# Kernel optimization log

Measured on AMD Instinct MI355X. Metric: run time of the kernel, lower is better.

The kernel has to match this reference:

```python
import jax, jax.numpy as jnp
import numpy as np

N = 100000      # nodes
E = 1600000     # edges (avg degree 16)
F_IN = 64       # in_channels
H = 64          # hidden_channels
L = 3           # num_layers
FINAL = H * L   # jk='cat'


def setup_inputs() -> dict:
    key = jax.random.key(0)
    ks = jax.random.split(key, 16)

    def w(k, i, o):
        return (jax.random.normal(k, (i, o), jnp.float32) / np.sqrt(i)).astype(jnp.float32)

    x = jax.random.normal(ks[0], (N, F_IN), jnp.float32)
    edge_index = jax.random.randint(ks[1], (2, E), 0, N, dtype=jnp.int32)

    inp = {
        'x': x,
        'edge_index': edge_index,
        # layer 1 (in -> H): lin_l (neighbors, with bias), lin_r (root, no bias)
        'W1l': w(ks[2], F_IN, H), 'b1': jnp.zeros((H,), jnp.float32), 'W1r': w(ks[3], F_IN, H),
        # layer 2 (H -> H)
        'W2l': w(ks[4], H, H), 'b2': jnp.zeros((H,), jnp.float32), 'W2r': w(ks[5], H, H),
        # layer 3 (H -> H)
        'W3l': w(ks[6], H, H), 'b3': jnp.zeros((H,), jnp.float32), 'W3r': w(ks[7], H, H),
        # final linear on JK-concat
        'Wlin': w(ks[8], FINAL, 1), 'blin': jnp.zeros((1,), jnp.float32),
    }
    return inp


def _sage_conv(x, src, dst, inv_deg, Wl, bl, Wr):
    # gather neighbor features along edges, segment-mean by destination node
    msg = x[src]                                             # [E, F]
    agg = jax.ops.segment_sum(msg, dst, num_segments=N)      # [N, F]
    agg = agg * inv_deg[:, None]                             # mean aggregation
    return agg @ Wl + bl + x @ Wr                            # lin_l(agg) + lin_r(x)


def reference(x, edge_index, W1l, b1, W1r, W2l, b2, W2r, W3l, b3, W3r, Wlin, blin):
    src, dst = edge_index[0], edge_index[1]
    deg = jax.ops.segment_sum(jnp.ones((E,), jnp.float32), dst, num_segments=N)
    inv_deg = 1.0 / jnp.maximum(deg, 1.0)

    xs = []
    h = x
    for (Wl, bl, Wr) in ((W1l, b1, W1r), (W2l, b2, W2r), (W3l, b3, W3r)):
        h = jax.nn.relu(_sage_conv(h, src, dst, inv_deg, Wl, bl, Wr))
        # dropout is identity in eval mode
        xs.append(h)

    hcat = jnp.concatenate(xs, axis=-1)   # JK 'cat' -> [N, H*L]
    out = hcat @ Wlin + blin              # [N, 1]
    return jax.nn.sigmoid(out).reshape(-1)
```

## Files before the change

kernel.cpp:

```cpp
#include <hip/hip_runtime.h>
#include <math.h>

#define N_NODES 100000
#define N_EDGES 1600000
#define HD 64
#define TILE 128
#define NBUCK 128
#define BNODES 1024
#define EPB 4096
#define EPB2 8192
#define HB 196

typedef unsigned short ushort_t;
typedef unsigned char uchar_t;
typedef __attribute__((ext_vector_type(8))) unsigned short ushort8_t;
typedef __attribute__((ext_vector_type(8))) short short8_t;
typedef __attribute__((ext_vector_type(4))) float float4_t;
typedef __attribute__((ext_vector_type(2))) float float2_t;

__device__ __forceinline__ float bf2f(ushort_t h){
  union{unsigned u; float f;} v; v.u = ((unsigned)h)<<16; return v.f;
}
__device__ __forceinline__ ushort_t f2bf(float f){
  union{float f; unsigned u;} v; v.f=f;
  unsigned b = v.u + 0x7FFF + ((v.u>>16)&1);
  return (ushort_t)(b>>16);
}
__device__ __forceinline__ void acc8(float* acc, unsigned ux, unsigned uy, float m){
  float2_t f;
  f=__builtin_amdgcn_cvt_pk_f32_fp8((int)ux,false); acc[0]=fmaf(m,f.x,acc[0]); acc[1]=fmaf(m,f.y,acc[1]);
  f=__builtin_amdgcn_cvt_pk_f32_fp8((int)ux,true ); acc[2]=fmaf(m,f.x,acc[2]); acc[3]=fmaf(m,f.y,acc[3]);
  f=__builtin_amdgcn_cvt_pk_f32_fp8((int)uy,false); acc[4]=fmaf(m,f.x,acc[4]); acc[5]=fmaf(m,f.y,acc[5]);
  f=__builtin_amdgcn_cvt_pk_f32_fp8((int)uy,true ); acc[6]=fmaf(m,f.x,acc[6]); acc[7]=fmaf(m,f.y,acc[7]);
}

__global__ __launch_bounds__(512) void k_convert_hist(
    const float* __restrict__ in, ushort_t* __restrict__ obf, uchar_t* __restrict__ o8,
    const int* __restrict__ dst, int* __restrict__ bcnt2d, int nfeat, int nedge){
  __shared__ int lh[NBUCK];
  int t=threadIdx.x, b=blockIdx.x;
  bool doHist = (b < HB);
  if(doHist){
    if(t<NBUCK) lh[t]=0;
    __syncthreads();
    int base=b*EPB2;
    #pragma unroll
    for(int j=0;j<16;j++){
      int e=base+t+j*512;
      if(e<nedge) atomicAdd(&lh[dst[e]>>10],1);
    }
  }
  int idx = (b*512+t)*4;
  if(idx+3<nfeat){
    float4 v = *(const float4*)&in[idx];
    ushort2 a; a.x=f2bf(v.x); a.y=f2bf(v.y);
    ushort2 c2; c2.x=f2bf(v.z); c2.y=f2bf(v.w);
    *(ushort2*)&obf[idx] = a;
    *(ushort2*)&obf[idx+2] = c2;
    int p = __builtin_amdgcn_cvt_pk_fp8_f32(v.x, v.y, 0, false);
    p     = __builtin_amdgcn_cvt_pk_fp8_f32(v.z, v.w, p, true);
    *(unsigned int*)&o8[idx] = (unsigned int)p;
  } else {
    for(int k=idx;k<nfeat;k++){
      obf[k]=f2bf(in[k]);
      int p = __builtin_amdgcn_cvt_pk_fp8_f32(in[k], 0.f, 0, false);
      o8[k] = (uchar_t)(p & 0xFF);
    }
  }
  if(doHist){
    __syncthreads();
    if(t<NBUCK) bcnt2d[b*NBUCK+t]=lh[t];
  }
}

__global__ void k_scan128(const int* __restrict__ bcnt2d, int* __restrict__ gcur, int* __restrict__ gbase){
  __shared__ int s[NBUCK];
  int t=threadIdx.x;
  int v=0;
  int b=0;
  for(; b+4<=HB; b+=4)
    v += bcnt2d[b*NBUCK+t] + bcnt2d[(b+1)*NBUCK+t] + bcnt2d[(b+2)*NBUCK+t] + bcnt2d[(b+3)*NBUCK+t];
  for(; b<HB; ++b) v += bcnt2d[b*NBUCK+t];
  s[t]=v;
  __syncthreads();
  for(int off=1; off<NBUCK; off<<=1){
    int a=(t>=off)? s[t-off]:0;
    __syncthreads();
    s[t]+=a;
    __syncthreads();
  }
  int excl = s[t]-v;
  gcur[t]=excl;
  gbase[t]=excl;
  if(t==NBUCK-1) gbase[NBUCK]=s[t];
}

__global__ __launch_bounds__(512) void k_reorder(
    const int* __restrict__ src, const int* __restrict__ dst,
    int* __restrict__ gcur, int* __restrict__ pairs, int n){
  __shared__ int lh[NBUCK];
  __shared__ int lbase[NBUCK];
  int t=threadIdx.x;
  if(t<NBUCK) lh[t]=0;
  __syncthreads();
  int base = blockIdx.x*EPB;
  int bb[8], rr[8], pv[8];
  #pragma unroll
  for(int j=0;j<8;j++){
    int e = base + t + j*512;
    if(e<n){
      int d=dst[e];
      int b=d>>10;
      rr[j]=atomicAdd(&lh[b],1);
      bb[j]=b;
      pv[j]=src[e] | ((d & 1023)<<17);
    } else bb[j]=-1;
  }
  __syncthreads();
  if(t<NBUCK && lh[t]) lbase[t]=atomicAdd(&gcur[t], lh[t]);
  __syncthreads();
  #pragma unroll
  for(int j=0;j<8;j++){
    if(bb[j]>=0){
      int pos = lbase[bb[j]] + rr[j];
      pairs[pos] = pv[j];
    }
  }
}

__global__ __launch_bounds__(512) void k_bucket_csr(
    const int* __restrict__ pairs, const int* __restrict__ gbase,
    int* __restrict__ rowptr, float* __restrict__ invdeg,
    int* __restrict__ csr, int nnodes, int nedges){
  __shared__ int cnt[BNODES];
  __shared__ int part[512];
  int t=threadIdx.x, b=blockIdx.x;
  int nb0 = b*BNODES;
  int e0 = gbase[b], e1 = gbase[b+1];
  cnt[t]=0; cnt[t+512]=0;
  __syncthreads();
  for(int e=e0+t; e<e1; e+=512) atomicAdd(&cnt[pairs[e]>>17], 1);
  __syncthreads();
  int c0 = cnt[2*t], c1 = cnt[2*t+1];
  part[t] = c0+c1;
  __syncthreads();
  for(int off=1; off<512; off<<=1){
    int a=(t>=off)? part[t-off]:0;
    __syncthreads();
    part[t]+=a;
    __syncthreads();
  }
  int base = part[t]-(c0+c1);
  int ex0 = base, ex1 = base+c0;
  int n_0 = nb0+2*t, n_1 = nb0+2*t+1;
  if(n_0<nnodes){ rowptr[n_0]=e0+ex0; invdeg[n_0]=1.0f/fmaxf((float)c0,1.0f); }
  if(n_1<nnodes){ rowptr[n_1]=e0+ex1; invdeg[n_1]=1.0f/fmaxf((float)c1,1.0f); }
  if(b==0 && t==0) rowptr[nnodes]=nedges;
  cnt[2*t]=ex0; cnt[2*t+1]=ex1;
  __syncthreads();
  for(int e=e0+t; e<e1; e+=512){
    int p = pairs[e];
    int pos = atomicAdd(&cnt[p>>17], 1);
    csr[e0+pos] = p & 0x1FFFF;
  }
}

__global__ __launch_bounds__(512) void k_gather(
    const uchar_t* __restrict__ hin8, ushort_t* __restrict__ agg,
    const int* __restrict__ rowptr, const int* __restrict__ csr,
    const float* __restrict__ invdeg, int nnodes)
{
  int t=threadIdx.x;
  int lane=t&63, wid=t>>6;
  int nA=(blockIdx.x*8+wid)*2;
  if(nA>=nnodes) return;
  int nB=nA+1;
  bool hasB = (nB<nnodes);
  int slot=lane>>3, c=lane&7;
  int rA0=rowptr[nA], rA1=rowptr[nA+1];
  int rB0=rA1, rB1=hasB? rowptr[nB+1] : rA1;
  float idgA=invdeg[nA];
  float idgB=hasB? invdeg[nB] : 0.f;
  float aA[8]={0,0,0,0,0,0,0,0}, aB[8]={0,0,0,0,0,0,0,0};
  int ca=(rA1>rA0)? rA1-1 : 0;
  int cb=(rB1>rB0)? rB1-1 : 0;

  {
    int i1=rA0+slot, i2=rA0+8+slot;
    int j1=rB0+slot, j2=rB0+8+slot;
    int sA1=csr[min(i1,ca)], sA2=csr[min(i2,ca)];
    int sB1=csr[min(j1,cb)], sB2=csr[min(j2,cb)];
    uint2 uA1=*(const uint2*)&hin8[(size_t)sA1*HD + c*8];
    uint2 uA2=*(const uint2*)&hin8[(size_t)sA2*HD + c*8];
    uint2 uB1=*(const uint2*)&hin8[(size_t)sB1*HD + c*8];
    uint2 uB2=*(const uint2*)&hin8[(size_t)sB2*HD + c*8];
    acc8(aA,uA1.x,uA1.y,(i1<rA1)?1.f:0.f);
    acc8(aA,uA2.x,uA2.y,(i2<rA1)?1.f:0.f);
    acc8(aB,uB1.x,uB1.y,(j1<rB1)?1.f:0.f);
    acc8(aB,uB2.x,uB2.y,(j2<rB1)?1.f:0.f);
  }
  int eA=rA0+16, eB=rB0+16;
  for(; eA<rA1 && eB<rB1; eA+=16, eB+=16){
    int i1=eA+slot, i2=eA+8+slot;
    int j1=eB+slot, j2=eB+8+slot;
    int sA1=csr[min(i1,ca)], sA2=csr[min(i2,ca)];
    int sB1=csr[min(j1,cb)], sB2=csr[min(j2,cb)];
    uint2 uA1=*(const uint2*)&hin8[(size_t)sA1*HD + c*8];
    uint2 uA2=*(const uint2*)&hin8[(size_t)sA2*HD + c*8];
    uint2 uB1=*(const uint2*)&hin8[(size_t)sB1*HD + c*8];
    uint2 uB2=*(const uint2*)&hin8[(size_t)sB2*HD + c*8];
    acc8(aA,uA1.x,uA1.y,(i1<rA1)?1.f:0.f);
    acc8(aA,uA2.x,uA2.y,(i2<rA1)?1.f:0.f);
    acc8(aB,uB1.x,uB1.y,(j1<rB1)?1.f:0.f);
    acc8(aB,uB2.x,uB2.y,(j2<rB1)?1.f:0.f);
  }
  for(; eA<rA1; eA+=16){
    int i1=eA+slot, i2=eA+8+slot;
    int s1=csr[min(i1,ca)], s2=csr[min(i2,ca)];
    uint2 u1=*(const uint2*)&hin8[(size_t)s1*HD + c*8];
    uint2 u2=*(const uint2*)&hin8[(size_t)s2*HD + c*8];
    acc8(aA,u1.x,u1.y,(i1<rA1)?1.f:0.f);
    acc8(aA,u2.x,u2.y,(i2<rA1)?1.f:0.f);
  }
  for(; eB<rB1; eB+=16){
    int i1=eB+slot, i2=eB+8+slot;
    int s1=csr[min(i1,cb)], s2=csr[min(i2,cb)];
    uint2 u1=*(const uint2*)&hin8[(size_t)s1*HD + c*8];
    uint2 u2=*(const uint2*)&hin8[(size_t)s2*HD + c*8];
    acc8(aB,u1.x,u1.y,(i1<rB1)?1.f:0.f);
    acc8(aB,u2.x,u2.y,(i2<rB1)?1.f:0.f);
  }
  #pragma unroll
  for(int off=8; off<64; off<<=1){
    #pragma unroll
    for(int j=0;j<8;j++){
      aA[j] += __shfl_xor(aA[j], off, 64);
      aB[j] += __shfl_xor(aB[j], off, 64);
    }
  }
  if(slot==0){
    ushort8_t o;
    #pragma unroll
    for(int j=0;j<8;j++) o[j] = f2bf(aA[j]*idgA);
    *(ushort8_t*)&agg[(size_t)nA*HD + c*8] = o;
    if(hasB){
      #pragma unroll
      for(int j=0;j<8;j++) o[j] = f2bf(aB[j]*idgB);
      *(ushort8_t*)&agg[(size_t)nB*HD + c*8] = o;
    }
  }
}

__global__ __launch_bounds__(256) void k_dense(
    const ushort_t* __restrict__ hin, const ushort_t* __restrict__ agg,
    ushort_t* __restrict__ hout, uchar_t* __restrict__ h8out,
    const float* __restrict__ Wl, const float* __restrict__ bvec, const float* __restrict__ Wr,
    const float* __restrict__ wseg, const float* __restrict__ blin,
    float* __restrict__ partial, float* __restrict__ finout,
    int first, int nnodes)
{
  __shared__ ushort_t sWt[64][136];
  __shared__ ushort_t sOut[TILE][72];
  __shared__ float sB[64], sS[64];
  int t = threadIdx.x;
  int n0 = blockIdx.x*TILE;

  {
    int col = t & 63;
    int k0  = (t >> 6) * 32;
    #pragma unroll
    for (int j = 0; j < 32; ++j) {
      int k = k0 + j;
      float wv = (k < 64) ? Wl[k*64 + col] : Wr[(k-64)*64 + col];
      sWt[col][k] = f2bf(wv);
    }
  }
  if(t<64){ sB[t]=bvec[t]; sS[t]=wseg[t]; }
  __syncthreads();

  int lane = t & 63, wv_ = t >> 6;
  int r16 = lane & 15, g4 = lane >> 4;
  int nbase = n0 + wv_*32;

  float4_t acc[2][4];
  #pragma unroll
  for(int mt=0;mt<2;mt++)
    #pragma unroll
    for(int ct=0;ct<4;ct++)
      #pragma unroll
      for(int r=0;r<4;r++) acc[mt][ct][r]=0.f;

  #pragma unroll
  for (int ks = 0; ks < 4; ++ks) {
    const ushort_t* abuf = (ks < 2) ? agg : hin;
    int koff = (ks & 1)*32 + g4*8;
    short8_t aF[2];
    #pragma unroll
    for (int mt = 0; mt < 2; ++mt) {
      int node = nbase + mt*16 + r16;
      if (node >= nnodes) node = nnodes-1;
      aF[mt] = *(const short8_t*)&abuf[(size_t)node*HD + koff];
    }
    #pragma unroll
    for (int ct = 0; ct < 4; ++ct) {
      short8_t bF = *(const short8_t*)&sWt[ct*16 + r16][ks*32 + g4*8];
      acc[0][ct] = __builtin_amdgcn_mfma_f32_16x16x32_bf16(aF[0], bF, acc[0][ct], 0,0,0);
      acc[1][ct] = __builtin_amdgcn_mfma_f32_16x16x32_bf16(aF[1], bF, acc[1][ct], 0,0,0);
    }
  }

  #pragma unroll
  for (int mt = 0; mt < 2; ++mt)
    #pragma unroll
    for (int ct = 0; ct < 4; ++ct) {
      int col = ct*16 + r16;
      #pragma unroll
      for (int r = 0; r < 4; ++r) {
        int row = g4*4 + r;
        float v = fmaxf(acc[mt][ct][r] + sB[col], 0.f);
        sOut[wv_*32 + mt*16 + row][col] = f2bf(v);
      }
    }
  __syncthreads();

  {
    int nl = t >> 1, half = t & 1;
    int node = n0 + nl;
    float p = 0.f;
    #pragma unroll
    for (int i = 0; i < 4; ++i) {
      int c0 = half*32 + i*8;
      ushort8_t v = *(const ushort8_t*)&sOut[nl][c0];
      float fv[8];
      #pragma unroll
      for (int j = 0; j < 8; ++j){ fv[j]=bf2f(v[j]); p = fmaf(fv[j], sS[c0+j], p); }
      if (!finout && node < nnodes){
        *(ushort8_t*)&hout[(size_t)node*HD + c0] = v;
        int q0 = __builtin_amdgcn_cvt_pk_fp8_f32(fv[0], fv[1], 0, false);
        q0     = __builtin_amdgcn_cvt_pk_fp8_f32(fv[2], fv[3], q0, true);
        int q1 = __builtin_amdgcn_cvt_pk_fp8_f32(fv[4], fv[5], 0, false);
        q1     = __builtin_amdgcn_cvt_pk_fp8_f32(fv[6], fv[7], q1, true);
        uint2 st; st.x=(unsigned)q0; st.y=(unsigned)q1;
        *(uint2*)&h8out[(size_t)node*HD + c0] = st;
      }
    }
    p += __shfl_xor(p, 1, 64);
    if (half == 0 && node < nnodes) {
      float q = first ? (blin[0] + p) : (partial[node] + p);
      if (finout) finout[node] = 1.0f/(1.0f+expf(-q));
      else partial[node] = q;
    }
  }
}

extern "C" void kernel_launch(void* const* d_in, const int* in_sizes, int n_in,
                              void* d_out, int out_size, void* d_ws, size_t ws_size,
                              hipStream_t stream){
  const float* x    =(const float*)d_in[0];
  const int*   ei   =(const int*)  d_in[1];
  const float* W1l  =(const float*)d_in[2];
  const float* b1   =(const float*)d_in[3];
  const float* W1r  =(const float*)d_in[4];
  const float* W2l  =(const float*)d_in[5];
  const float* b2   =(const float*)d_in[6];
  const float* W2r  =(const float*)d_in[7];
  const float* W3l  =(const float*)d_in[8];
  const float* b3   =(const float*)d_in[9];
  const float* W3r  =(const float*)d_in[10];
  const float* Wlin =(const float*)d_in[11];
  const float* blin =(const float*)d_in[12];
  float* out=(float*)d_out;

  const int N=N_NODES, E=N_EDGES;
  char* ws=(char*)d_ws;
  size_t off=0;
  auto take=[&](size_t bytes)->char*{ char* p=ws+off; off=(off+bytes+255)&~(size_t)255; return p; };
  int*      bcnt2d   =(int*)     take((size_t)HB*NBUCK*4);
  int*      gcur     =(int*)     take((size_t)NBUCK*4);
  int*      gbase    =(int*)     take((size_t)(NBUCK+1)*4);
  int*      rowptr   =(int*)     take((size_t)(N+1)*4);
  int*      csr      =(int*)     take((size_t)E*4);
  int*      pairs    =(int*)     take((size_t)E*4);
  float*    invdeg   =(float*)   take((size_t)N*4);
  ushort_t* xbf      =(ushort_t*)take((size_t)N*HD*2);
  ushort_t* hbfA     =(ushort_t*)take((size_t)N*HD*2);
  ushort_t* hbfB     =(ushort_t*)take((size_t)N*HD*2);
  ushort_t* aggbf    =(ushort_t*)take((size_t)N*HD*2);
  uchar_t*  x8       =(uchar_t*) take((size_t)N*HD);
  uchar_t*  h8A      =(uchar_t*) take((size_t)N*HD);
  uchar_t*  h8B      =(uchar_t*) take((size_t)N*HD);
  float*    pacc     =(float*)   take((size_t)N*4);

  const int RB=(E+EPB-1)/EPB;
  const int CB=(N*HD/4+511)/512;
  const int BB=(N+BNODES-1)/BNODES;

  k_convert_hist<<<CB, 512, 0, stream>>>(x, xbf, x8, ei+E, bcnt2d, N*HD, E);
  k_scan128     <<<1, NBUCK, 0, stream>>>(bcnt2d, gcur, gbase);
  k_reorder     <<<RB, 512, 0, stream>>>(ei, ei+E, gcur, pairs, E);
  k_bucket_csr  <<<BB, 512, 0, stream>>>(pairs, gbase, rowptr, invdeg, csr, N, E);

  dim3 gg((N+15)/16);
  dim3 gd((N+TILE-1)/TILE);

  k_gather<<<gg, 512, 0, stream>>>(x8,  aggbf, rowptr, csr, invdeg, N);
  k_dense <<<gd, 256, 0, stream>>>(xbf,  aggbf, hbfA, h8A, W1l,b1,W1r, Wlin+0,   blin, pacc, (float*)nullptr, 1, N);
  k_gather<<<gg, 512, 0, stream>>>(h8A, aggbf, rowptr, csr, invdeg, N);
  k_dense <<<gd, 256, 0, stream>>>(hbfA, aggbf, hbfB, h8B, W2l,b2,W2r, Wlin+64,  blin, pacc, (float*)nullptr, 0, N);
  k_gather<<<gg, 512, 0, stream>>>(h8B, aggbf, rowptr, csr, invdeg, N);
  k_dense <<<gd, 256, 0, stream>>>(hbfB, aggbf, hbfA, h8A, W3l,b3,W3r, Wlin+128, blin, pacc, out, 0, N);
}
```

Measured before the change: 196.8 us.

## Fuse neighbor gather with dense SAGE layer and pre-convert weights once

Merges the per-layer gather kernel and the dense MFMA kernel into one kernel. Each 512-thread block aggregates 16 nodes into shared memory, then four waves run the 16-row bf16 MFMA, apply ReLU and the JK partial dot. This removes the global round trip for the aggregated features and three kernel launches. Weight transposition and bf16 conversion move to a single prep kernel that writes all layers once, so blocks only copy them into shared memory. In exchange, each small block reloads 16KB of weights, and only 4 of 8 waves do MFMA work.

```diff
diff --git a/kernel.cpp b/kernel.cpp
--- a/kernel.cpp
+++ b/kernel.cpp
@@ -4,7 +4,6 @@
 #define N_NODES 100000
 #define N_EDGES 1600000
 #define HD 64
-#define TILE 128
 #define NBUCK 128
 #define BNODES 1024
 #define EPB 4096
@@ -14,6 +13,7 @@
 typedef unsigned short ushort_t;
 typedef unsigned char uchar_t;
 typedef __attribute__((ext_vector_type(8))) unsigned short ushort8_t;
+typedef __attribute__((ext_vector_type(4))) unsigned short ushort4_t;
 typedef __attribute__((ext_vector_type(8))) short short8_t;
 typedef __attribute__((ext_vector_type(4))) float float4_t;
 typedef __attribute__((ext_vector_type(2))) float float2_t;
@@ -73,6 +73,26 @@
   }
 }
 
+__global__ void k_prep_w(const float* __restrict__ W1l, const float* __restrict__ W1r,
+                         const float* __restrict__ W2l, const float* __restrict__ W2r,
+                         const float* __restrict__ W3l, const float* __restrict__ W3r,
+                         ushort_t* __restrict__ wt){
+  int idx = blockIdx.x*512 + threadIdx.x;
+  int layer = idx>>11;
+  int rem = idx & 2047;
+  int col = rem >> 5;
+  int kg = rem & 31;
+  const float* Wl = layer==0? W1l : (layer==1? W2l : W3l);
+  const float* Wr = layer==0? W1r : (layer==1? W2r : W3r);
+  ushort_t* o = wt + layer*8192 + col*128 + kg*4;
+  #pragma unroll
+  for(int i=0;i<4;i++){
+    int k = kg*4+i;
+    float v = (k<64)? Wl[k*64+col] : Wr[(k-64)*64+col];
+    o[i]=f2bf(v);
+  }
+}
+
 __global__ void k_scan128(const int* __restrict__ bcnt2d, int* __restrict__ gcur, int* __restrict__ gbase){
   __shared__ int s[NBUCK];
   int t=threadIdx.x;
@@ -165,190 +185,158 @@
   }
 }
 
-__global__ __launch_bounds__(512) void k_gather(
-    const uchar_t* __restrict__ hin8, ushort_t* __restrict__ agg,
-    const int* __restrict__ rowptr, const int* __restrict__ csr,
-    const float* __restrict__ invdeg, int nnodes)
+__global__ __launch_bounds__(512) void k_fused(
+    const ushort_t* __restrict__ hin, const uchar_t* __restrict__ hin8,
+    const ushort_t* __restrict__ wt,
+    const float* __restrict__ bvec, const float* __restrict__ wseg, const float* __restrict__ blin,
+    const int* __restrict__ rowptr, const int* __restrict__ csr, const float* __restrict__ invdeg,
+    ushort_t* __restrict__ hout, uchar_t* __restrict__ h8out,
+    float* __restrict__ pacc, float* __restrict__ finout, int first, int nnodes)
 {
+  __shared__ __align__(16) ushort_t sWt[64][136];
+  __shared__ __align__(16) ushort_t sAgg[16][72];
+  __shared__ __align__(16) ushort_t sOut[16][72];
+  __shared__ float sB[64], sS[64];
   int t=threadIdx.x;
-  int lane=t&63, wid=t>>6;
-  int nA=(blockIdx.x*8+wid)*2;
-  if(nA>=nnodes) return;
-  int nB=nA+1;
-  bool hasB = (nB<nnodes);
-  int slot=lane>>3, c=lane&7;
-  int rA0=rowptr[nA], rA1=rowptr[nA+1];
-  int rB0=rA1, rB1=hasB? rowptr[nB+1] : rA1;
-  float idgA=invdeg[nA];
-  float idgB=hasB? invdeg[nB] : 0.f;
-  float aA[8]={0,0,0,0,0,0,0,0}, aB[8]={0,0,0,0,0,0,0,0};
-  int ca=(rA1>rA0)? rA1-1 : 0;
-  int cb=(rB1>rB0)? rB1-1 : 0;
+  int n0=blockIdx.x*16;
 
   {
-    int i1=rA0+slot, i2=rA0+8+slot;
-    int j1=rB0+slot, j2=rB0+8+slot;
-    int sA1=csr[min(i1,ca)], sA2=csr[min(i2,ca)];
-    int sB1=csr[min(j1,cb)], sB2=csr[min(j2,cb)];
-    uint2 uA1=*(const uint2*)&hin8[(size_t)sA1*HD + c*8];
-    uint2 uA2=*(const uint2*)&hin8[(size_t)sA2*HD + c*8];
-    uint2 uB1=*(const uint2*)&hin8[(size_t)sB1*HD + c*8];
-    uint2 uB2=*(const uint2*)&hin8[(size_t)sB2*HD + c*8];
-    acc8(aA,uA1.x,uA1.y,(i1<rA1)?1.f:0.f);
-    acc8(aA,uA2.x,uA2.y,(i2<rA1)?1.f:0.f);
-    acc8(aB,uB1.x,uB1.y,(j1<rB1)?1.f:0.f);
-    acc8(aB,uB2.x,uB2.y,(j2<rB1)?1.f:0.f);
-  }
-  int eA=rA0+16, eB=rB0+16;
-  for(; eA<rA1 && eB<rB1; eA+=16, eB+=16){
-    int i1=eA+slot, i2=eA+8+slot;
-    int j1=eB+slot, j2=eB+8+slot;
-    int sA1=csr[min(i1,ca)], sA2=csr[min(i2,ca)];
-    int sB1=csr[min(j1,cb)], sB2=csr[min(j2,cb)];
-    uint2 uA1=*(const uint2*)&hin8[(size_t)sA1*HD + c*8];
-    uint2 uA2=*(const uint2*)&hin8[(size_t)sA2*HD + c*8];
-    uint2 uB1=*(const uint2*)&hin8[(size_t)sB1*HD + c*8];
-    uint2 uB2=*(const uint2*)&hin8[(size_t)sB2*HD + c*8];
-    acc8(aA,uA1.x,uA1.y,(i1<rA1)?1.f:0.f);
-    acc8(aA,uA2.x,uA2.y,(i2<rA1)?1.f:0.f);
-    acc8(aB,uB1.x,uB1.y,(j1<rB1)?1.f:0.f);
-    acc8(aB,uB2.x,uB2.y,(j2<rB1)?1.f:0.f);
-  }
-  for(; eA<rA1; eA+=16){
-    int i1=eA+slot, i2=eA+8+slot;
-    int s1=csr[min(i1,ca)], s2=csr[min(i2,ca)];
-    uint2 u1=*(const uint2*)&hin8[(size_t)s1*HD + c*8];
-    uint2 u2=*(const uint2*)&hin8[(size_t)s2*HD + c*8];
-    acc8(aA,u1.x,u1.y,(i1<rA1)?1.f:0.f);
-    acc8(aA,u2.x,u2.y,(i2<rA1)?1.f:0.f);
-  }
-  for(; eB<rB1; eB+=16){
-    int i1=eB+slot, i2=eB+8+slot;
-    int s1=csr[min(i1,cb)], s2=csr[min(i2,cb)];
-    uint2 u1=*(const uint2*)&hin8[(size_t)s1*HD + c*8];
-    uint2 u2=*(const uint2*)&hin8[(size_t)s2*HD + c*8];
-    acc8(aB,u1.x,u1.y,(i1<rB1)?1.f:0.f);
-    acc8(aB,u2.x,u2.y,(i2<rB1)?1.f:0.f);
-  }
-  #pragma unroll
-  for(int off=8; off<64; off<<=1){
+    int col=t>>3, sub=t&7;
+    const ushort8_t* src=(const ushort8_t*)(wt + col*128);
+    ushort8_t* dst=(ushort8_t*)&sWt[col][0];
+    dst[sub*2]   = src[sub*2];
+    dst[sub*2+1] = src[sub*2+1];
+  }
+  if(t<64){ sB[t]=bvec[t]; sS[t]=wseg[t]; }
+
+  {
+    int lane=t&63, wid=t>>6;
+    int nA=n0+wid*2, nB=nA+1;
+    if(nA<nnodes){
+      bool hasB=(nB<nnodes);
+      int slot=lane>>3, c=lane&7;
+      int rA0=rowptr[nA], rA1=rowptr[nA+1];
+      int rB0=rA1, rB1=hasB? rowptr[nB+1] : rA1;
+      float idgA=invdeg[nA];
+      float idgB=hasB? invdeg[nB] : 0.f;
+      float aA[8]={0,0,0,0,0,0,0,0}, aB[8]={0,0,0,0,0,0,0,0};
+      int ca=(rA1>rA0)? rA1-1 : 0;
+      int cb=(rB1>rB0)? rB1-1 : 0;
+      {
+        int i1=rA0+slot, i2=rA0+8+slot;
+        int j1=rB0+slot, j2=rB0+8+slot;
+        int sA1=csr[min(i1,ca)], sA2=csr[min(i2,ca)];
+        int sB1=csr[min(j1,cb)], sB2=csr[min(j2,cb)];
+        uint2 uA1=*(const uint2*)&hin8[(size_t)sA1*HD + c*8];
+        uint2 uA2=*(const uint2*)&hin8[(size_t)sA2*HD + c*8];
+        uint2 uB1=*(const uint2*)&hin8[(size_t)sB1*HD + c*8];
+        uint2 uB2=*(const uint2*)&hin8[(size_t)sB2*HD + c*8];
+        acc8(aA,uA1.x,uA1.y,(i1<rA1)?1.f:0.f);
+        acc8(aA,uA2.x,uA2.y,(i2<rA1)?1.f:0.f);
+        acc8(aB,uB1.x,uB1.y,(j1<rB1)?1.f:0.f);
+        acc8(aB,uB2.x,uB2.y,(j2<rB1)?1.f:0.f);
+      }
+      int eA=rA0+16, eB=rB0+16;
+      for(; eA<rA1 && eB<rB1; eA+=16, eB+=16){
+        int i1=eA+slot, i2=eA+8+slot;
+        int j1=eB+slot, j2=eB+8+slot;
+        int sA1=csr[min(i1,ca)], sA2=csr[min(i2,ca)];
+        int sB1=csr[min(j1,cb)], sB2=csr[min(j2,cb)];
+        uint2 uA1=*(const uint2*)&hin8[(size_t)sA1*HD + c*8];
+        uint2 uA2=*(const uint2*)&hin8[(size_t)sA2*HD + c*8];
+        uint2 uB1=*(const uint2*)&hin8[(size_t)sB1*HD + c*8];
+        uint2 uB2=*(const uint2*)&hin8[(size_t)sB2*HD + c*8];
+        acc8(aA,uA1.x,uA1.y,(i1<rA1)?1.f:0.f);
+        acc8(aA,uA2.x,uA2.y,(i2<rA1)?1.f:0.f);
+        acc8(aB,uB1.x,uB1.y,(j1<rB1)?1.f:0.f);
+        acc8(aB,uB2.x,uB2.y,(j2<rB1)?1.f:0.f);
+      }
+      for(; eA<rA1; eA+=16){
+        int i1=eA+slot, i2=eA+8+slot;
+        int s1=csr[min(i1,ca)], s2=csr[min(i2,ca)];
+        uint2 u1=*(const uint2*)&hin8[(size_t)s1*HD + c*8];
+        uint2 u2=*(const uint2*)&hin8[(size_t)s2*HD + c*8];
+        acc8(aA,u1.x,u1.y,(i1<rA1)?1.f:0.f);
+        acc8(aA,u2.x,u2.y,(i2<rA1)?1.f:0.f);
+      }
+      for(; eB<rB1; eB+=16){
+        int i1=eB+slot, i2=eB+8+slot;
+        int s1=csr[min(i1,cb)], s2=csr[min(i2,cb)];
+        uint2 u1=*(const uint2*)&hin8[(size_t)s1*HD + c*8];
+        uint2 u2=*(const uint2*)&hin8[(size_t)s2*HD + c*8];
+        acc8(aB,u1.x,u1.y,(i1<rB1)?1.f:0.f);
+        acc8(aB,u2.x,u2.y,(i2<rB1)?1.f:0.f);
+      }
+      #pragma unroll
+      for(int off=8; off<64; off<<=1){
+        #pragma unroll
+        for(int j=0;j<8;j++){
+          aA[j] += __shfl_xor(aA[j], off, 64);
+          aB[j] += __shfl_xor(aB[j], off, 64);
+        }
+      }
+      if(slot==0){
+        ushort8_t o;
+        #pragma unroll
+        for(int j=0;j<8;j++) o[j] = f2bf(aA[j]*idgA);
+        *(ushort8_t*)&sAgg[wid*2][c*8] = o;
+        if(hasB){
+          #pragma unroll
+          for(int j=0;j<8;j++) o[j] = f2bf(aB[j]*idgB);
+          *(ushort8_t*)&sAgg[wid*2+1][c*8] = o;
+        }
+      }
+    }
+  }
+  __syncthreads();
+
+  {
+    int wv = t>>6;
+    if(wv<4){
+      int lane=t&63, r16=lane&15, g4=lane>>4;
+      float4_t acc = {0.f,0.f,0.f,0.f};
+      #pragma unroll
+      for(int ks=0; ks<4; ++ks){
+        short8_t aF;
+        if(ks<2){
+          aF = *(const short8_t*)&sAgg[r16][ks*32 + g4*8];
+        } else {
+          int node = n0 + r16;
+          if(node >= nnodes) node = nnodes-1;
+          aF = *(const short8_t*)&hin[(size_t)node*HD + (ks&1)*32 + g4*8];
+        }
+        short8_t bF = *(const short8_t*)&sWt[wv*16 + r16][ks*32 + g4*8];
+        acc = __builtin_amdgcn_mfma_f32_16x16x32_bf16(aF, bF, acc, 0,0,0);
+      }
+      int col = wv*16 + r16;
+      #pragma unroll
+      for(int r=0;r<4;r++){
+        int nl = g4*4 + r;
+        float v = fmaxf(acc[r] + sB[col], 0.f);
+        sOut[nl][col] = f2bf(v);
+      }
+    }
+  }
+  __syncthreads();
+
+  if(t<256){
+    int nl=t>>4, j=t&15, c0=j*4;
+    int node=n0+nl;
+    ushort4_t v = *(const ushort4_t*)&sOut[nl][c0];
+    float f0=bf2f(v[0]), f1=bf2f(v[1]), f2v=bf2f(v[2]), f3=bf2f(v[3]);
+    float p = f0*sS[c0] + f1*sS[c0+1] + f2v*sS[c0+2] + f3*sS[c0+3];
+    if(!finout && node<nnodes){
+      *(ushort4_t*)&hout[(size_t)node*HD + c0] = v;
+      int q = __builtin_amdgcn_cvt_pk_fp8_f32(f0, f1, 0, false);
+      q     = __builtin_amdgcn_cvt_pk_fp8_f32(f2v, f3, q, true);
+      *(unsigned*)&h8out[(size_t)node*HD + c0] = (unsigned)q;
+    }
     #pragma unroll
-    for(int j=0;j<8;j++){
-      aA[j] += __shfl_xor(aA[j], off, 64);
-      aB[j] += __shfl_xor(aB[j], off, 64);
-    }
-  }
-  if(slot==0){
-    ushort8_t o;
-    #pragma unroll
-    for(int j=0;j<8;j++) o[j] = f2bf(aA[j]*idgA);
-    *(ushort8_t*)&agg[(size_t)nA*HD + c*8] = o;
-    if(hasB){
-      #pragma unroll
-      for(int j=0;j<8;j++) o[j] = f2bf(aB[j]*idgB);
-      *(ushort8_t*)&agg[(size_t)nB*HD + c*8] = o;
-    }
-  }
-}
-
-__global__ __launch_bounds__(256) void k_dense(
-    const ushort_t* __restrict__ hin, const ushort_t* __restrict__ agg,
-    ushort_t* __restrict__ hout, uchar_t* __restrict__ h8out,
-    const float* __restrict__ Wl, const float* __restrict__ bvec, const float* __restrict__ Wr,
-    const float* __restrict__ wseg, const float* __restrict__ blin,
-    float* __restrict__ partial, float* __restrict__ finout,
-    int first, int nnodes)
-{
-  __shared__ ushort_t sWt[64][136];
-  __shared__ ushort_t sOut[TILE][72];
-  __shared__ float sB[64], sS[64];
-  int t = threadIdx.x;
-  int n0 = blockIdx.x*TILE;
-
-  {
-    int col = t & 63;
-    int k0  = (t >> 6) * 32;
-    #pragma unroll
-    for (int j = 0; j < 32; ++j) {
-      int k = k0 + j;
-      float wv = (k < 64) ? Wl[k*64 + col] : Wr[(k-64)*64 + col];
-      sWt[col][k] = f2bf(wv);
-    }
-  }
-  if(t<64){ sB[t]=bvec[t]; sS[t]=wseg[t]; }
-  __syncthreads();
-
-  int lane = t & 63, wv_ = t >> 6;
-  int r16 = lane & 15, g4 = lane >> 4;
-  int nbase = n0 + wv_*32;
-
-  float4_t acc[2][4];
-  #pragma unroll
-  for(int mt=0;mt<2;mt++)
-    #pragma unroll
-    for(int ct=0;ct<4;ct++)
-      #pragma unroll
-      for(int r=0;r<4;r++) acc[mt][ct][r]=0.f;
-
-  #pragma unroll
-  for (int ks = 0; ks < 4; ++ks) {
-    const ushort_t* abuf = (ks < 2) ? agg : hin;
-    int koff = (ks & 1)*32 + g4*8;
-    short8_t aF[2];
-    #pragma unroll
-    for (int mt = 0; mt < 2; ++mt) {
-      int node = nbase + mt*16 + r16;
-      if (node >= nnodes) node = nnodes-1;
-      aF[mt] = *(const short8_t*)&abuf[(size_t)node*HD + koff];
-    }
-    #pragma unroll
-    for (int ct = 0; ct < 4; ++ct) {
-      short8_t bF = *(const short8_t*)&sWt[ct*16 + r16][ks*32 + g4*8];
-      acc[0][ct] = __builtin_amdgcn_mfma_f32_16x16x32_bf16(aF[0], bF, acc[0][ct], 0,0,0);
-      acc[1][ct] = __builtin_amdgcn_mfma_f32_16x16x32_bf16(aF[1], bF, acc[1][ct], 0,0,0);
-    }
-  }
-
-  #pragma unroll
-  for (int mt = 0; mt < 2; ++mt)
-    #pragma unroll
-    for (int ct = 0; ct < 4; ++ct) {
-      int col = ct*16 + r16;
-      #pragma unroll
-      for (int r = 0; r < 4; ++r) {
-        int row = g4*4 + r;
-        float v = fmaxf(acc[mt][ct][r] + sB[col], 0.f);
-        sOut[wv_*32 + mt*16 + row][col] = f2bf(v);
-      }
-    }
-  __syncthreads();
-
-  {
-    int nl = t >> 1, half = t & 1;
-    int node = n0 + nl;
-    float p = 0.f;
-    #pragma unroll
-    for (int i = 0; i < 4; ++i) {
-      int c0 = half*32 + i*8;
-      ushort8_t v = *(const ushort8_t*)&sOut[nl][c0];
-      float fv[8];
-      #pragma unroll
-      for (int j = 0; j < 8; ++j){ fv[j]=bf2f(v[j]); p = fmaf(fv[j], sS[c0+j], p); }
-      if (!finout && node < nnodes){
-        *(ushort8_t*)&hout[(size_t)node*HD + c0] = v;
-        int q0 = __builtin_amdgcn_cvt_pk_fp8_f32(fv[0], fv[1], 0, false);
-        q0     = __builtin_amdgcn_cvt_pk_fp8_f32(fv[2], fv[3], q0, true);
-        int q1 = __builtin_amdgcn_cvt_pk_fp8_f32(fv[4], fv[5], 0, false);
-        q1     = __builtin_amdgcn_cvt_pk_fp8_f32(fv[6], fv[7], q1, true);
-        uint2 st; st.x=(unsigned)q0; st.y=(unsigned)q1;
-        *(uint2*)&h8out[(size_t)node*HD + c0] = st;
-      }
-    }
-    p += __shfl_xor(p, 1, 64);
-    if (half == 0 && node < nnodes) {
-      float q = first ? (blin[0] + p) : (partial[node] + p);
-      if (finout) finout[node] = 1.0f/(1.0f+expf(-q));
-      else partial[node] = q;
+    for(int off=1; off<16; off<<=1) p += __shfl_xor(p, off, 16);
+    if(j==0 && node<nnodes){
+      float q = first ? (blin[0]+p) : (pacc[node]+p);
+      if(finout) finout[node] = 1.0f/(1.0f+expf(-q));
+      else pacc[node] = q;
     }
   }
 }
@@ -382,10 +370,10 @@
   int*      csr      =(int*)     take((size_t)E*4);
   int*      pairs    =(int*)     take((size_t)E*4);
   float*    invdeg   =(float*)   take((size_t)N*4);
+  ushort_t* wt3      =(ushort_t*)take((size_t)3*8192*2);
   ushort_t* xbf      =(ushort_t*)take((size_t)N*HD*2);
   ushort_t* hbfA     =(ushort_t*)take((size_t)N*HD*2);
   ushort_t* hbfB     =(ushort_t*)take((size_t)N*HD*2);
-  ushort_t* aggbf    =(ushort_t*)take((size_t)N*HD*2);
   uchar_t*  x8       =(uchar_t*) take((size_t)N*HD);
   uchar_t*  h8A      =(uchar_t*) take((size_t)N*HD);
   uchar_t*  h8B      =(uchar_t*) take((size_t)N*HD);
@@ -396,17 +384,14 @@
   const int BB=(N+BNODES-1)/BNODES;
 
   k_convert_hist<<<CB, 512, 0, stream>>>(x, xbf, x8, ei+E, bcnt2d, N*HD, E);
+  k_prep_w      <<<12, 512, 0, stream>>>(W1l,W1r,W2l,W2r,W3l,W3r, wt3);
   k_scan128     <<<1, NBUCK, 0, stream>>>(bcnt2d, gcur, gbase);
   k_reorder     <<<RB, 512, 0, stream>>>(ei, ei+E, gcur, pairs, E);
   k_bucket_csr  <<<BB, 512, 0, stream>>>(pairs, gbase, rowptr, invdeg, csr, N, E);
 
-  dim3 gg((N+15)/16);
-  dim3 gd((N+TILE-1)/TILE);
-
-  k_gather<<<gg, 512, 0, stream>>>(x8,  aggbf, rowptr, csr, invdeg, N);
-  k_dense <<<gd, 256, 0, stream>>>(xbf,  aggbf, hbfA, h8A, W1l,b1,W1r, Wlin+0,   blin, pacc, (float*)nullptr, 1, N);
-  k_gather<<<gg, 512, 0, stream>>>(h8A, aggbf, rowptr, csr, invdeg, N);
-  k_dense <<<gd, 256, 0, stream>>>(hbfA, aggbf, hbfB, h8B, W2l,b2,W2r, Wlin+64,  blin, pacc, (float*)nullptr, 0, N);
-  k_gather<<<gg, 512, 0, stream>>>(h8B, aggbf, rowptr, csr, invdeg, N);
-  k_dense <<<gd, 256, 0, stream>>>(hbfB, aggbf, hbfA, h8A, W3l,b3,W3r, Wlin+128, blin, pacc, out, 0, N);
-}
+  dim3 gf((N+15)/16);
+
+  k_fused<<<gf, 512, 0, stream>>>(xbf,  x8,  wt3,        b1, Wlin+0,   blin, rowptr, csr, invdeg, hbfA, h8A, pacc, (float*)nullptr, 1, N);
+  k_fused<<<gf, 512, 0, stream>>>(hbfA, h8A, wt3+8192,   b2, Wlin+64,  blin, rowptr, csr, invdeg, hbfB, h8B, pacc, (float*)nullptr, 0, N);
+  k_fused<<<gf, 512, 0, stream>>>(hbfB, h8B, wt3+16384,  b3, Wlin+128, blin, rowptr, csr, invdeg, hbfA, h8A, pacc, out, 0, N);
+}
```

Result: no change. 198.4 us (+0.8%).
